# Performance work log

Measured on AMD Instinct MI355X. Metric: run time of the kernel, lower is better.

## Reference

```python
import jax, jax.numpy as jnp
import numpy as np

L, B, T, IN, D, H, FF, C = 6, 4, 1024, 256, 1024, 16, 4096, 10
HD = D // H
EPS = 1e-5


def _ln(x, g, b):
    mu = jnp.mean(x, axis=-1, keepdims=True)
    var = jnp.var(x, axis=-1, keepdims=True)
    return (x - mu) * jax.lax.rsqrt(var + EPS) * g + b


def setup_inputs() -> dict:
    key = jax.random.key(0)
    ks = jax.random.split(key, 10)
    s = 0.02
    rn = lambda k, shape: jax.random.normal(k, shape, jnp.float32) * s
    return {
        "x": jax.random.normal(ks[0], (B, T, IN), jnp.float32),
        "input_w": rn(ks[1], (D, IN)), "input_b": jnp.zeros((D,), jnp.float32),
        "Wqkv": rn(ks[2], (L, 3 * D, D)), "bqkv": jnp.zeros((L, 3 * D), jnp.float32),
        "Wo": rn(ks[3], (L, D, D)), "bo": jnp.zeros((L, D), jnp.float32),
        "ln1_g": jnp.ones((L, D), jnp.float32), "ln1_b": jnp.zeros((L, D), jnp.float32),
        "ln2_g": jnp.ones((L, D), jnp.float32), "ln2_b": jnp.zeros((L, D), jnp.float32),
        "W1": rn(ks[4], (L, FF, D)), "b1": jnp.zeros((L, FF), jnp.float32),
        "W2": rn(ks[5], (L, D, FF)), "b2": jnp.zeros((L, D), jnp.float32),
        "head_w": rn(ks[6], (C, D)), "head_b": jnp.zeros((C,), jnp.float32),
    }


def reference(x, input_w, input_b, Wqkv, bqkv, Wo, bo, ln1_g, ln1_b, ln2_g, ln2_b, W1, b1, W2, b2, head_w, head_b):
    Bx, Tx, _ = x.shape
    # input projection (torch Linear layout: [out,in])
    h = jnp.einsum('bti,di->btd', x, input_w) + input_b
    # ALiBi bias: mean slope across heads, additive |i-j| distance penalty
    slopes = 2.0 ** (-8.0 * jnp.arange(1, H + 1, dtype=jnp.float32) / H)
    slope = slopes.mean()
    idx = jnp.arange(Tx, dtype=jnp.float32)
    alibi = -slope * jnp.abs(idx[:, None] - idx[None, :])  # (T,T), same for every head
    scale = 1.0 / np.sqrt(HD)
    for l in range(L):
        qkv = jnp.einsum('btd,ed->bte', h, Wqkv[l]) + bqkv[l]
        q, k, v = jnp.split(qkv, 3, axis=-1)
        q = q.reshape(Bx, Tx, H, HD)
        k = k.reshape(Bx, Tx, H, HD)
        v = v.reshape(Bx, Tx, H, HD)
        scores = jnp.einsum('bthd,bshd->bhts', q, k) * scale + alibi
        attn = jax.nn.softmax(scores, axis=-1)
        o = jnp.einsum('bhts,bshd->bthd', attn, v).reshape(Bx, Tx, D)
        o = jnp.einsum('btd,ed->bte', o, Wo[l]) + bo[l]
        h = _ln(h + o, ln1_g[l], ln1_b[l])  # post-norm
        ff = jax.nn.relu(jnp.einsum('btd,fd->btf', h, W1[l]) + b1[l])
        ff = jnp.einsum('btf,df->btd', ff, W2[l]) + b2[l]
        h = _ln(h + ff, ln2_g[l], ln2_b[l])
    last = h[:, -1, :]
    return jnp.einsum('bd,cd->bc', last, head_w) + head_b
```

## Files before the change

kernel.cpp:

```cpp
#include <hip/hip_runtime.h>
#include <cmath>

#define D_MODEL 1024
#define N_HEADS 16
#define HEAD_DIM 64
#define SEQ 1024
#define BATCH 4
#define FF_DIM 4096
#define IN_DIM 256
#define N_LAYERS 6
#define N_CLS 10

typedef __bf16 bf16x8 __attribute__((ext_vector_type(8)));
typedef __bf16 bf16x4 __attribute__((ext_vector_type(4)));
typedef float f32x4 __attribute__((ext_vector_type(4)));
typedef unsigned short u16x8 __attribute__((ext_vector_type(8)));

__device__ __forceinline__ unsigned short f2bf(float f) {
    unsigned int u = __float_as_uint(f);
    u += 0x7fffu + ((u >> 16) & 1u);
    return (unsigned short)(u >> 16);
}
__device__ __forceinline__ float bf2f(unsigned short u) {
    return __uint_as_float((unsigned int)u << 16);
}
__device__ __forceinline__ float fexp2(float x) {
    return __builtin_amdgcn_exp2f(x);
}

__device__ __forceinline__ void gll16(const void* g, void* l) {
    __builtin_amdgcn_global_load_lds((const __attribute__((address_space(1))) void*)g,
                                     (__attribute__((address_space(3))) void*)l, 16, 0, 0);
}

__global__ __launch_bounds__(256)
void cvt_f32_bf16(const float* __restrict__ src, unsigned short* __restrict__ dst, int n) {
    int i = (blockIdx.x * 256 + threadIdx.x) * 4;
    if (i + 4 <= n) {
        float4 v = *(const float4*)(src + i);
        ushort4 o;
        o.x = f2bf(v.x); o.y = f2bf(v.y); o.z = f2bf(v.z); o.w = f2bf(v.w);
        *(ushort4*)(dst + i) = o;
    }
}

#define WQKV_SZ (3 * D_MODEL * D_MODEL)
#define WO_SZ   (D_MODEL * D_MODEL)
#define W1_SZ   (FF_DIM * D_MODEL)
#define W2_SZ   (D_MODEL * FF_DIM)
__global__ __launch_bounds__(256)
void cvt_layer(const float* __restrict__ wq, const float* __restrict__ wo,
               const float* __restrict__ w1, const float* __restrict__ w2,
               unsigned short* __restrict__ dq, unsigned short* __restrict__ dvo,
               unsigned short* __restrict__ d1, unsigned short* __restrict__ d2)
{
    int i = (blockIdx.x * 256 + threadIdx.x) * 4;
    const float* s; unsigned short* d; int off;
    if (i < WQKV_SZ)                    { s = wq; d = dq;  off = i; }
    else if (i < WQKV_SZ + WO_SZ)       { s = wo; d = dvo; off = i - WQKV_SZ; }
    else if (i < WQKV_SZ + WO_SZ + W1_SZ) { s = w1; d = d1; off = i - WQKV_SZ - WO_SZ; }
    else                                { s = w2; d = d2;  off = i - WQKV_SZ - WO_SZ - W1_SZ; }
    float4 v = *(const float4*)(s + off);
    ushort4 o;
    o.x = f2bf(v.x); o.y = f2bf(v.y); o.z = f2bf(v.z); o.w = f2bf(v.w);
    *(ushort4*)(d + off) = o;
}

template<int MU, bool LOADB, bool GATE, typename F>
__device__ __forceinline__
void gphase(f32x4 (&acc)[8][4], bf16x8 (&bfr)[4],
            const unsigned short* slabA, const unsigned short* slabB,
            const int (&aoff)[2][4], const int (&boff)[4], F&& stage, bool gate0)
{
    bf16x8 afr[4];
    if (LOADB) {
        _Pragma("unroll")
        for (int n = 0; n < 4; ++n) bfr[n] = *(const bf16x8*)(slabB + boff[n]);
    }
    _Pragma("unroll")
    for (int m = 0; m < 4; ++m) afr[m] = *(const bf16x8*)(slabA + aoff[MU][m]);
    stage();
    __builtin_amdgcn_s_barrier();
    asm volatile("s_waitcnt lgkmcnt(0)" ::: "memory");
    __builtin_amdgcn_sched_barrier(0);
    __builtin_amdgcn_s_setprio(1);
    _Pragma("unroll")
    for (int m = 0; m < 4; ++m)
        _Pragma("unroll")
        for (int n = 0; n < 4; ++n)
            acc[MU * 4 + m][n] =
                __builtin_amdgcn_mfma_f32_16x16x32_bf16(afr[m], bfr[n], acc[MU * 4 + m][n], 0, 0, 0);
    __builtin_amdgcn_s_setprio(0);
    if (GATE) {
        if (gate0) asm volatile("s_waitcnt vmcnt(0)" ::: "memory");
        else       asm volatile("s_waitcnt vmcnt(4)" ::: "memory");
    }
    __builtin_amdgcn_s_barrier();
}

__global__ __launch_bounds__(512, 2)
void gemm256(const unsigned short* __restrict__ A, const unsigned short* __restrict__ B,
             const float* __restrict__ bias,
             float* __restrict__ Cf, unsigned short* __restrict__ Cb,
             int N, int lda, int klen, int relu, size_t slab_stride)
{
    extern __shared__ unsigned short lds[];
    auto slA = [&](int buf, int kh) { return lds + (buf * 2 + kh) * 8192; };
    auto slB = [&](int buf, int kh) { return lds + 32768 + (buf * 2 + kh) * 8192; };

    const int nbc = N >> 8;
    const int nwg = gridDim.x;
    const int orig = blockIdx.x;
    const int xcd = orig & 7, lid = orig >> 3;
    const int q = nwg >> 3, r = nwg & 7;
    const int wgid = (xcd < r ? xcd * (q + 1) : r * (q + 1) + (xcd - r) * q) + lid;
    const int brow = wgid / nbc, bcol = wgid % nbc;
    const int kpart = blockIdx.y;

    const int tid = threadIdx.x;
    const int w = tid >> 6, l = tid & 63;
    const int wr = w >> 2, wc = w & 3;
    const int lr = l & 15, lg4 = l >> 4;

    const unsigned short* Ab = A + (size_t)brow * 256 * lda + (size_t)kpart * klen;
    const unsigned short* Bb = B + (size_t)bcol * 256 * lda + (size_t)kpart * klen;
    float* Cfp = Cf;
    unsigned short* Cbp = Cb ? Cb + (size_t)kpart * slab_stride : nullptr;
    const float* biasp = (kpart == 0) ? bias : nullptr;

    const int G0 = w * 128 + l;
    const int tr0 = G0 >> 2;
    const int lg0 = (G0 & 3) ^ ((tr0 >> 1) & 3);

    auto stA = [&](int buf, int kh, int tile) {
        unsigned short* d = slA(buf, kh) + G0 * 8;
        const unsigned short* s = Ab + (size_t)tr0 * lda + tile * 64 + kh * 32 + lg0 * 8;
        gll16(s, d);
        gll16(s + (size_t)16 * lda, d + 512);
    };
    auto stB = [&](int buf, int kh, int tile) {
        unsigned short* d = slB(buf, kh) + G0 * 8;
        const unsigned short* s = Bb + (size_t)tr0 * lda + tile * 64 + kh * 32 + lg0 * 8;
        gll16(s, d);
        gll16(s + (size_t)16 * lda, d + 512);
    };

    int aoff[2][4], boff[4];
    #pragma unroll
    for (int mu = 0; mu < 2; ++mu)
        #pragma unroll
        for (int m = 0; m < 4; ++m) {
            int tA = wr * 128 + mu * 64 + m * 16 + lr;
            aoff[mu][m] = tA * 32 + ((lg4 ^ ((tA >> 1) & 3)) << 3);
        }
    #pragma unroll
    for (int n = 0; n < 4; ++n) {
        int tB = wc * 64 + n * 16 + lr;
        boff[n] = tB * 32 + ((lg4 ^ ((tB >> 1) & 3)) << 3);
    }

    f32x4 acc[8][4] = {};

    const int KT = klen >> 6;
    stA(0, 0, 0); stA(0, 1, 0); stB(0, 0, 0); stB(0, 1, 0);
    if (KT > 1) { stA(1, 0, 1); stA(1, 1, 1); stB(1, 0, 1); stB(1, 1, 1); }
    asm volatile("s_waitcnt vmcnt(0)" ::: "memory");
    __builtin_amdgcn_s_barrier();

    for (int I = 0; I < KT / 2; ++I) {
        const int t2 = 2 * I;
        const bool s12 = (I > 0);
        const bool more = (t2 + 2 < KT);
        bf16x8 bfr[4];
        gphase<0, true , false>(acc, bfr, slA(0,0), slB(0,0), aoff, boff, [&]{ if (s12)  stA(1,1,t2+1); }, false);
        gphase<1, false, false>(acc, bfr, slA(0,0), slB(0,0), aoff, boff, [&]{ if (s12)  stB(1,1,t2+1); }, false);
        gphase<0, true , false>(acc, bfr, slA(0,1), slB(0,1), aoff, boff, [&]{ if (more) stA(0,0,t2+2); }, false);
        gphase<1, false, true >(acc, bfr, slA(0,1), slB(0,1), aoff, boff, [&]{ if (more) stB(0,0,t2+2); }, !more);
        gphase<0, true , false>(acc, bfr, slA(1,0), slB(1,0), aoff, boff, [&]{ if (more) stA(0,1,t2+2); }, false);
        gphase<1, false, false>(acc, bfr, slA(1,0), slB(1,0), aoff, boff, [&]{ if (more) stB(0,1,t2+2); }, false);
        gphase<0, true , false>(acc, bfr, slA(1,1), slB(1,1), aoff, boff, [&]{ if (more) stA(1,0,t2+3); }, false);
        gphase<1, false, true >(acc, bfr, slA(1,1), slB(1,1), aoff, boff, [&]{ if (more) stB(1,0,t2+3); }, !more);
    }

    const int crow0 = brow * 256 + wr * 128;
    const int ccol0 = bcol * 256 + wc * 64;
    #pragma unroll
    for (int n = 0; n < 4; ++n) {
        int col = ccol0 + n * 16 + lr;
        float bv = biasp ? biasp[col] : 0.0f;
        #pragma unroll
        for (int m = 0; m < 8; ++m) {
            int row0 = crow0 + m * 16 + lg4 * 4;
            #pragma unroll
            for (int j = 0; j < 4; ++j) {
                float v = acc[m][n][j] + bv;
                if (relu) v = fmaxf(v, 0.0f);
                size_t idx = (size_t)(row0 + j) * N + col;
                if (Cfp) Cfp[idx] = v;
                if (Cbp) Cbp[idx] = f2bf(v);
            }
        }
    }
}

__global__ __launch_bounds__(256, 2)
void attn_alibi(const unsigned short* __restrict__ qkv,
                unsigned short* __restrict__ out,
                float slope2)
{
    const int bid = blockIdx.x;
    const int id = (bid & 7) * 128 + (bid >> 3);
    const int qt = id & 15;
    const int bh = id >> 4;
    const int h  = bh & (N_HEADS - 1);
    const int b  = bh >> 4;
    const int w  = threadIdx.x >> 6, l = threadIdx.x & 63;
    const int lr = l & 15, lg = l >> 4;

    __shared__ __align__(16) unsigned short lsK[64 * 64];
    __shared__ __align__(16) unsigned short lsVt[64 * 64];
    __shared__ __align__(16) unsigned short lsP[4 * 16 * 64];

    const size_t rs = 3 * D_MODEL;
    const unsigned short* base = qkv + (size_t)b * SEQ * rs;
    const int qrow_w = qt * 64 + w * 16;
    const float c1 = 0.125f * 1.4426950408889634f;

    bf16x8 aq[2];
    #pragma unroll
    for (int ks = 0; ks < 2; ++ks)
        aq[ks] = *(const bf16x8*)(base + (size_t)(qrow_w + lr) * rs + h * HEAD_DIM + ks * 32 + lg * 8);

    float m_run = -1e30f, s_run = 0.f;
    f32x4 oacc[4] = {};
    const float qi = (float)(qrow_w + lr);

    for (int kt = 0; kt < SEQ / 64; ++kt) {
        #pragma unroll
        for (int i = 0; i < 2; ++i) {
            int chunk = i * 4 + w;
            int e = chunk * 512 + l * 8;
            int row = e >> 6, c = e & 63;
            int gcol = c ^ ((row & 7) << 3);
            gll16(base + (size_t)(kt * 64 + row) * rs + D_MODEL + h * HEAD_DIM + gcol,
                  &lsK[chunk * 512]);
        }
        #pragma unroll
        for (int i = 0; i < 2; ++i) {
            int oct = i * 4 + w;
            int kj  = l;
            u16x8 v = *(const u16x8*)(base + (size_t)(kt * 64 + kj) * rs + 2 * D_MODEL + h * HEAD_DIM + oct * 8);
            #pragma unroll
            for (int jj = 0; jj < 8; ++jj) {
                int row = oct * 8 + jj;
                lsVt[row * 64 + (kj ^ ((row & 7) << 3))] = v[jj];
            }
        }
        __syncthreads();

        f32x4 sacc[4] = {};
        #pragma unroll
        for (int ks = 0; ks < 2; ++ks) {
            #pragma unroll
            for (int n = 0; n < 4; ++n) {
                int row = n * 16 + lr;
                bf16x8 bk = *(const bf16x8*)&lsK[row * 64 + ((ks * 32 + lg * 8) ^ ((row & 7) << 3))];
                sacc[n] = __builtin_amdgcn_mfma_f32_16x16x32_bf16(bk, aq[ks], sacc[n], 0, 0, 0);
            }
        }

        float mx = -1e30f;
        #pragma unroll
        for (int n = 0; n < 4; ++n)
            #pragma unroll
            for (int jj = 0; jj < 4; ++jj) {
                float kjf = (float)(kt * 64 + n * 16 + lg * 4 + jj);
                float v = fmaf(sacc[n][jj], c1, -slope2 * fabsf(qi - kjf));
                sacc[n][jj] = v;
                mx = fmaxf(mx, v);
            }
        mx = fmaxf(mx, __shfl_xor(mx, 16));
        mx = fmaxf(mx, __shfl_xor(mx, 32));
        if (__any(mx > m_run + 8.0f)) {
            float mnew = fmaxf(m_run, mx);
            float corr = fexp2(m_run - mnew);
            m_run = mnew;
            s_run *= corr;
            #pragma unroll
            for (int j = 0; j < 4; ++j) {
                float cj = __shfl(corr, lg * 4 + j);
                #pragma unroll
                for (int nd = 0; nd < 4; ++nd)
                    oacc[nd][j] *= cj;
            }
        }
        float psum = 0.f;
        #pragma unroll
        for (int n = 0; n < 4; ++n)
            #pragma unroll
            for (int jj = 0; jj < 4; ++jj) {
                float p = fexp2(sacc[n][jj] - m_run);
                sacc[n][jj] = p;
                psum += p;
            }
        psum += __shfl_xor(psum, 16);
        psum += __shfl_xor(psum, 32);
        s_run += psum;

        #pragma unroll
        for (int n = 0; n < 4; ++n) {
            bf16x4 pk;
            pk[0] = (__bf16)sacc[n][0]; pk[1] = (__bf16)sacc[n][1];
            pk[2] = (__bf16)sacc[n][2]; pk[3] = (__bf16)sacc[n][3];
            *(bf16x4*)&lsP[w * 1024 + lr * 64 + ((n * 16 + lg * 4) ^ ((lr & 7) << 3))] = pk;
        }

        #pragma unroll
        for (int ks = 0; ks < 2; ++ks) {
            bf16x8 ap = *(const bf16x8*)&lsP[w * 1024 + lr * 64 + ((ks * 32 + lg * 8) ^ ((lr & 7) << 3))];
            #pragma unroll
            for (int nd = 0; nd < 4; ++nd) {
                int row = nd * 16 + lr;
                bf16x8 bv = *(const bf16x8*)&lsVt[row * 64 + ((ks * 32 + lg * 8) ^ ((row & 7) << 3))];
                oacc[nd] = __builtin_amdgcn_mfma_f32_16x16x32_bf16(ap, bv, oacc[nd], 0, 0, 0);
            }
        }
        __syncthreads();
    }

    float inv = 1.0f / s_run;
    #pragma unroll
    for (int j = 0; j < 4; ++j) {
        float invj = __shfl(inv, lg * 4 + j);
        int qrow = qrow_w + lg * 4 + j;
        #pragma unroll
        for (int nd = 0; nd < 4; ++nd) {
            int d = nd * 16 + lr;
            out[((size_t)b * SEQ + qrow) * D_MODEL + h * HEAD_DIM + d] = f2bf(oacc[nd][j] * invj);
        }
    }
}

__global__ __launch_bounds__(256)
void add_ln(const unsigned short* __restrict__ resid, const unsigned short* __restrict__ delta,
            size_t slab, int nslab,
            const float* __restrict__ g, const float* __restrict__ beta,
            unsigned short* __restrict__ out_b)
{
    const int row = blockIdx.x;
    const int t = threadIdx.x;
    const int w = t >> 6, l = t & 63;
    __shared__ float red[8];
    const size_t off = (size_t)row * D_MODEL + t * 4;

    ushort4 rv = *(const ushort4*)(resid + off);
    float x0 = bf2f(rv.x), x1 = bf2f(rv.y), x2 = bf2f(rv.z), x3 = bf2f(rv.w);
    for (int p = 0; p < nslab; ++p) {
        ushort4 dv = *(const ushort4*)(delta + p * slab + off);
        x0 += bf2f(dv.x); x1 += bf2f(dv.y); x2 += bf2f(dv.z); x3 += bf2f(dv.w);
    }
    float s  = x0 + x1 + x2 + x3;
    float s2 = x0 * x0 + x1 * x1 + x2 * x2 + x3 * x3;
    #pragma unroll
    for (int d = 1; d < 64; d <<= 1) {
        s  += __shfl_xor(s, d);
        s2 += __shfl_xor(s2, d);
    }
    if (l == 0) { red[w] = s; red[4 + w] = s2; }
    __syncthreads();
    s  = red[0] + red[1] + red[2] + red[3];
    s2 = red[4] + red[5] + red[6] + red[7];
    float mu  = s * (1.0f / D_MODEL);
    float var = s2 * (1.0f / D_MODEL) - mu * mu;
    float rsq = rsqrtf(var + 1e-5f);

    float4 gv = *(const float4*)(g + t * 4);
    float4 bv = *(const float4*)(beta + t * 4);
    float y0 = (x0 - mu) * rsq * gv.x + bv.x;
    float y1 = (x1 - mu) * rsq * gv.y + bv.y;
    float y2 = (x2 - mu) * rsq * gv.z + bv.z;
    float y3 = (x3 - mu) * rsq * gv.w + bv.w;
    ushort4 ob; ob.x = f2bf(y0); ob.y = f2bf(y1); ob.z = f2bf(y2); ob.w = f2bf(y3);
    *(ushort4*)(out_b + off) = ob;
}

__global__ __launch_bounds__(256)
void head_kernel(const unsigned short* __restrict__ h, const float* __restrict__ hw,
                 const float* __restrict__ hb, float* __restrict__ out)
{
    const int wv = threadIdx.x >> 6, l = threadIdx.x & 63;
    const int c = blockIdx.x;
    const unsigned short* hr = h + ((size_t)wv * SEQ + (SEQ - 1)) * D_MODEL;
    const float* wc = hw + (size_t)c * D_MODEL;
    float s = 0.f;
    #pragma unroll
    for (int i = 0; i < 16; ++i) {
        int k = i * 64 + l;
        s += bf2f(hr[k]) * wc[k];
    }
    #pragma unroll
    for (int d = 1; d < 64; d <<= 1)
        s += __shfl_xor(s, d);
    if (l == 0) out[wv * N_CLS + c] = s + hb[c];
}

extern "C" void kernel_launch(void* const* d_in, const int* in_sizes, int n_in,
                              void* d_out, int out_size, void* d_ws, size_t ws_size,
                              hipStream_t stream)
{
    const float* x     = (const float*)d_in[0];
    const float* in_w  = (const float*)d_in[1];
    const float* in_b  = (const float*)d_in[2];
    const float* Wqkv  = (const float*)d_in[3];
    const float* bqkv  = (const float*)d_in[4];
    const float* Wo    = (const float*)d_in[5];
    const float* bo    = (const float*)d_in[6];
    const float* ln1g  = (const float*)d_in[7];
    const float* ln1b  = (const float*)d_in[8];
    const float* ln2g  = (const float*)d_in[9];
    const float* ln2b  = (const float*)d_in[10];
    const float* W1    = (const float*)d_in[11];
    const float* b1    = (const float*)d_in[12];
    const float* W2    = (const float*)d_in[13];
    const float* b2    = (const float*)d_in[14];
    const float* headw = (const float*)d_in[15];
    const float* headb = (const float*)d_in[16];
    float* out = (float*)d_out;

    (void)hipFuncSetAttribute((const void*)gemm256, hipFuncAttributeMaxDynamicSharedMemorySize, 131072);

    char* ws = (char*)d_ws;
    size_t off = 0;
    auto alloc = [&](size_t bytes) -> void* {
        void* p = ws + off;
        off += (bytes + 255) & ~(size_t)255;
        return p;
    };
    const int MT = BATCH * SEQ;
    const size_t SLAB = (size_t)MT * D_MODEL;

    unsigned short* x_bf   = (unsigned short*)alloc((size_t)MT * IN_DIM * 2);
    unsigned short* h_bf   = (unsigned short*)alloc(SLAB * 2);
    unsigned short* qkv_bf = (unsigned short*)alloc((size_t)MT * 3 * D_MODEL * 2);
    unsigned short* att_bf = (unsigned short*)alloc(SLAB * 2);
    unsigned short* ff_bf  = (unsigned short*)alloc((size_t)MT * FF_DIM * 2);
    unsigned short* tmp_bf = (unsigned short*)alloc(SLAB * 2 * 4);
    unsigned short* win_bf = (unsigned short*)alloc((size_t)D_MODEL * IN_DIM * 2);
    unsigned short* wq_bf  = (unsigned short*)alloc((size_t)WQKV_SZ * 2);
    unsigned short* wo_bf  = (unsigned short*)alloc((size_t)WO_SZ * 2);
    unsigned short* w1_bf  = (unsigned short*)alloc((size_t)W1_SZ * 2);
    unsigned short* w2_bf  = (unsigned short*)alloc((size_t)W2_SZ * 2);

    double ssum = 0.0;
    for (int i = 1; i <= N_HEADS; ++i) ssum += pow(2.0, -8.0 * i / N_HEADS);
    const float slope = (float)(ssum / N_HEADS);
    const float slope2 = slope * 1.4426950408889634f;

    auto cvt = [&](const float* s, unsigned short* d, int n) {
        cvt_f32_bf16<<<n / 1024, 256, 0, stream>>>(s, d, n);
    };

    cvt(x, x_bf, MT * IN_DIM);
    cvt(in_w, win_bf, D_MODEL * IN_DIM);
    gemm256<<<dim3(16 * 4, 1), 512, 131072, stream>>>(
        x_bf, win_bf, in_b, nullptr, h_bf, D_MODEL, IN_DIM, IN_DIM, 0, 0);

    const int CVT_BLKS = (WQKV_SZ + WO_SZ + W1_SZ + W2_SZ) / 1024;

    for (int layer = 0; layer < N_LAYERS; ++layer) {
        cvt_layer<<<CVT_BLKS, 256, 0, stream>>>(
            Wqkv + (size_t)layer * WQKV_SZ, Wo + (size_t)layer * WO_SZ,
            W1 + (size_t)layer * W1_SZ, W2 + (size_t)layer * W2_SZ,
            wq_bf, wo_bf, w1_bf, w2_bf);

        gemm256<<<dim3(16 * 12, 1), 512, 131072, stream>>>(
            h_bf, wq_bf, bqkv + (size_t)layer * 3 * D_MODEL,
            nullptr, qkv_bf, 3 * D_MODEL, D_MODEL, D_MODEL, 0, 0);

        attn_alibi<<<BATCH * N_HEADS * (SEQ / 64), 256, 0, stream>>>(qkv_bf, att_bf, slope2);

        gemm256<<<dim3(16 * 4, 4), 512, 131072, stream>>>(
            att_bf, wo_bf, bo + (size_t)layer * D_MODEL,
            nullptr, tmp_bf, D_MODEL, D_MODEL, D_MODEL / 4, 0, SLAB);

        add_ln<<<MT, 256, 0, stream>>>(h_bf, tmp_bf, SLAB, 4,
            ln1g + (size_t)layer * D_MODEL, ln1b + (size_t)layer * D_MODEL, h_bf);

        gemm256<<<dim3(16 * 16, 1), 512, 131072, stream>>>(
            h_bf, w1_bf, b1 + (size_t)layer * FF_DIM,
            nullptr, ff_bf, FF_DIM, D_MODEL, D_MODEL, 1, 0);

        gemm256<<<dim3(16 * 4, 4), 512, 131072, stream>>>(
            ff_bf, w2_bf, b2 + (size_t)layer * D_MODEL,
            nullptr, tmp_bf, D_MODEL, FF_DIM, FF_DIM / 4, 0, SLAB);

        add_ln<<<MT, 256, 0, stream>>>(h_bf, tmp_bf, SLAB, 4,
            ln2g + (size_t)layer * D_MODEL, ln2b + (size_t)layer * D_MODEL, h_bf);
    }

    head_kernel<<<N_CLS, 256, 0, stream>>>(h_bf, headw, headb, out);
}
```

Before: 1.435 ms.

## Process 128 query rows per attention block to reuse K/V tiles

Each attention workgroup now handles a 128-row query tile, with every wave owning two 16-row sub-tiles. This halves the grid size and doubles the work done per K/V tile loaded into shared memory, so each K and V tile is reused across twice as many query rows. The cost is more registers per thread (two sets of accumulators and softmax state) and a larger P buffer in LDS, which may reduce occupancy. Fewer blocks are also available to fill the GPU's compute units.

```diff
diff --git a/kernel.cpp b/kernel.cpp
--- a/kernel.cpp
+++ b/kernel.cpp
@@ -209,9 +209,9 @@
                 float slope2)
 {
     const int bid = blockIdx.x;
-    const int id = (bid & 7) * 128 + (bid >> 3);
-    const int qt = id & 15;
-    const int bh = id >> 4;
+    const int id = (bid & 7) * 64 + (bid >> 3);
+    const int qt = id & 7;
+    const int bh = id >> 3;
     const int h  = bh & (N_HEADS - 1);
     const int b  = bh >> 4;
     const int w  = threadIdx.x >> 6, l = threadIdx.x & 63;
@@ -219,21 +219,27 @@
 
     __shared__ __align__(16) unsigned short lsK[64 * 64];
     __shared__ __align__(16) unsigned short lsVt[64 * 64];
-    __shared__ __align__(16) unsigned short lsP[4 * 16 * 64];
+    __shared__ __align__(16) unsigned short lsP[4 * 32 * 64];
 
     const size_t rs = 3 * D_MODEL;
     const unsigned short* base = qkv + (size_t)b * SEQ * rs;
-    const int qrow_w = qt * 64 + w * 16;
+    const int qrow_w = qt * 128 + w * 32;
     const float c1 = 0.125f * 1.4426950408889634f;
 
-    bf16x8 aq[2];
-    #pragma unroll
-    for (int ks = 0; ks < 2; ++ks)
-        aq[ks] = *(const bf16x8*)(base + (size_t)(qrow_w + lr) * rs + h * HEAD_DIM + ks * 32 + lg * 8);
-
-    float m_run = -1e30f, s_run = 0.f;
-    f32x4 oacc[4] = {};
-    const float qi = (float)(qrow_w + lr);
+    bf16x8 aq[2][2];
+    #pragma unroll
+    for (int rt = 0; rt < 2; ++rt)
+        #pragma unroll
+        for (int ks = 0; ks < 2; ++ks)
+            aq[rt][ks] = *(const bf16x8*)(base + (size_t)(qrow_w + rt * 16 + lr) * rs
+                                          + h * HEAD_DIM + ks * 32 + lg * 8);
+
+    float m_run[2] = {-1e30f, -1e30f};
+    float s_run[2] = {0.f, 0.f};
+    f32x4 oacc[2][4] = {};
+    float qi[2];
+    qi[0] = (float)(qrow_w + lr);
+    qi[1] = (float)(qrow_w + 16 + lr);
 
     for (int kt = 0; kt < SEQ / 64; ++kt) {
         #pragma unroll
@@ -258,85 +264,98 @@
         }
         __syncthreads();
 
-        f32x4 sacc[4] = {};
+        f32x4 sacc[2][4] = {};
         #pragma unroll
         for (int ks = 0; ks < 2; ++ks) {
             #pragma unroll
             for (int n = 0; n < 4; ++n) {
                 int row = n * 16 + lr;
                 bf16x8 bk = *(const bf16x8*)&lsK[row * 64 + ((ks * 32 + lg * 8) ^ ((row & 7) << 3))];
-                sacc[n] = __builtin_amdgcn_mfma_f32_16x16x32_bf16(bk, aq[ks], sacc[n], 0, 0, 0);
-            }
-        }
-
-        float mx = -1e30f;
-        #pragma unroll
-        for (int n = 0; n < 4; ++n)
-            #pragma unroll
-            for (int jj = 0; jj < 4; ++jj) {
-                float kjf = (float)(kt * 64 + n * 16 + lg * 4 + jj);
-                float v = fmaf(sacc[n][jj], c1, -slope2 * fabsf(qi - kjf));
-                sacc[n][jj] = v;
-                mx = fmaxf(mx, v);
-            }
-        mx = fmaxf(mx, __shfl_xor(mx, 16));
-        mx = fmaxf(mx, __shfl_xor(mx, 32));
-        if (__any(mx > m_run + 8.0f)) {
-            float mnew = fmaxf(m_run, mx);
-            float corr = fexp2(m_run - mnew);
-            m_run = mnew;
-            s_run *= corr;
-            #pragma unroll
-            for (int j = 0; j < 4; ++j) {
-                float cj = __shfl(corr, lg * 4 + j);
                 #pragma unroll
-                for (int nd = 0; nd < 4; ++nd)
-                    oacc[nd][j] *= cj;
-            }
-        }
-        float psum = 0.f;
-        #pragma unroll
-        for (int n = 0; n < 4; ++n)
-            #pragma unroll
-            for (int jj = 0; jj < 4; ++jj) {
-                float p = fexp2(sacc[n][jj] - m_run);
-                sacc[n][jj] = p;
-                psum += p;
-            }
-        psum += __shfl_xor(psum, 16);
-        psum += __shfl_xor(psum, 32);
-        s_run += psum;
-
-        #pragma unroll
-        for (int n = 0; n < 4; ++n) {
-            bf16x4 pk;
-            pk[0] = (__bf16)sacc[n][0]; pk[1] = (__bf16)sacc[n][1];
-            pk[2] = (__bf16)sacc[n][2]; pk[3] = (__bf16)sacc[n][3];
-            *(bf16x4*)&lsP[w * 1024 + lr * 64 + ((n * 16 + lg * 4) ^ ((lr & 7) << 3))] = pk;
+                for (int rt = 0; rt < 2; ++rt)
+                    sacc[rt][n] = __builtin_amdgcn_mfma_f32_16x16x32_bf16(bk, aq[rt][ks], sacc[rt][n], 0, 0, 0);
+            }
+        }
+
+        #pragma unroll
+        for (int rt = 0; rt < 2; ++rt) {
+            float mx = -1e30f;
+            #pragma unroll
+            for (int n = 0; n < 4; ++n)
+                #pragma unroll
+                for (int jj = 0; jj < 4; ++jj) {
+                    float kjf = (float)(kt * 64 + n * 16 + lg * 4 + jj);
+                    float v = fmaf(sacc[rt][n][jj], c1, -slope2 * fabsf(qi[rt] - kjf));
+                    sacc[rt][n][jj] = v;
+                    mx = fmaxf(mx, v);
+                }
+            mx = fmaxf(mx, __shfl_xor(mx, 16));
+            mx = fmaxf(mx, __shfl_xor(mx, 32));
+            if (__any(mx > m_run[rt] + 8.0f)) {
+                float mnew = fmaxf(m_run[rt], mx);
+                float corr = fexp2(m_run[rt] - mnew);
+                m_run[rt] = mnew;
+                s_run[rt] *= corr;
+                #pragma unroll
+                for (int j = 0; j < 4; ++j) {
+                    float cj = __shfl(corr, lg * 4 + j);
+                    #pragma unroll
+                    for (int nd = 0; nd < 4; ++nd)
+                        oacc[rt][nd][j] *= cj;
+                }
+            }
+            float psum = 0.f;
+            #pragma unroll
+            for (int n = 0; n < 4; ++n)
+                #pragma unroll
+                for (int jj = 0; jj < 4; ++jj) {
+                    float p = fexp2(sacc[rt][n][jj] - m_run[rt]);
+                    sacc[rt][n][jj] = p;
+                    psum += p;
+                }
+            psum += __shfl_xor(psum, 16);
+            psum += __shfl_xor(psum, 32);
+            s_run[rt] += psum;
+
+            #pragma unroll
+            for (int n = 0; n < 4; ++n) {
+                bf16x4 pk;
+                pk[0] = (__bf16)sacc[rt][n][0]; pk[1] = (__bf16)sacc[rt][n][1];
+                pk[2] = (__bf16)sacc[rt][n][2]; pk[3] = (__bf16)sacc[rt][n][3];
+                *(bf16x4*)&lsP[w * 2048 + (rt * 16 + lr) * 64 + ((n * 16 + lg * 4) ^ ((lr & 7) << 3))] = pk;
+            }
         }
 
         #pragma unroll
         for (int ks = 0; ks < 2; ++ks) {
-            bf16x8 ap = *(const bf16x8*)&lsP[w * 1024 + lr * 64 + ((ks * 32 + lg * 8) ^ ((lr & 7) << 3))];
+            bf16x8 ap[2];
+            #pragma unroll
+            for (int rt = 0; rt < 2; ++rt)
+                ap[rt] = *(const bf16x8*)&lsP[w * 2048 + (rt * 16 + lr) * 64 + ((ks * 32 + lg * 8) ^ ((lr & 7) << 3))];
             #pragma unroll
             for (int nd = 0; nd < 4; ++nd) {
                 int row = nd * 16 + lr;
                 bf16x8 bv = *(const bf16x8*)&lsVt[row * 64 + ((ks * 32 + lg * 8) ^ ((row & 7) << 3))];
-                oacc[nd] = __builtin_amdgcn_mfma_f32_16x16x32_bf16(ap, bv, oacc[nd], 0, 0, 0);
+                #pragma unroll
+                for (int rt = 0; rt < 2; ++rt)
+                    oacc[rt][nd] = __builtin_amdgcn_mfma_f32_16x16x32_bf16(ap[rt], bv, oacc[rt][nd], 0, 0, 0);
             }
         }
         __syncthreads();
     }
 
-    float inv = 1.0f / s_run;
-    #pragma unroll
-    for (int j = 0; j < 4; ++j) {
-        float invj = __shfl(inv, lg * 4 + j);
-        int qrow = qrow_w + lg * 4 + j;
-        #pragma unroll
-        for (int nd = 0; nd < 4; ++nd) {
-            int d = nd * 16 + lr;
-            out[((size_t)b * SEQ + qrow) * D_MODEL + h * HEAD_DIM + d] = f2bf(oacc[nd][j] * invj);
+    #pragma unroll
+    for (int rt = 0; rt < 2; ++rt) {
+        float inv = 1.0f / s_run[rt];
+        #pragma unroll
+        for (int j = 0; j < 4; ++j) {
+            float invj = __shfl(inv, lg * 4 + j);
+            int qrow = qrow_w + rt * 16 + lg * 4 + j;
+            #pragma unroll
+            for (int nd = 0; nd < 4; ++nd) {
+                int d = nd * 16 + lr;
+                out[((size_t)b * SEQ + qrow) * D_MODEL + h * HEAD_DIM + d] = f2bf(oacc[rt][nd][j] * invj);
+            }
         }
     }
 }
@@ -477,7 +496,7 @@
             h_bf, wq_bf, bqkv + (size_t)layer * 3 * D_MODEL,
             nullptr, qkv_bf, 3 * D_MODEL, D_MODEL, D_MODEL, 0, 0);
 
-        attn_alibi<<<BATCH * N_HEADS * (SEQ / 64), 256, 0, stream>>>(qkv_bf, att_bf, slope2);
+        attn_alibi<<<BATCH * N_HEADS * (SEQ / 128), 256, 0, stream>>>(qkv_bf, att_bf, slope2);
 
         gemm256<<<dim3(16 * 4, 4), 512, 131072, stream>>>(
             att_bf, wo_bf, bo + (size_t)layer * D_MODEL,
```

Measured after the change: 1.427 ms. Within noise of the previous version (-0.5%).
